# Kernel tuning notes

Measured on AMD Instinct MI355X. Metric: run time of the kernel, lower is better.

The kernel has to match this reference:

```python
import jax, jax.numpy as jnp
import numpy as np

BN_EPS = 1e-5


def _bn(x, gamma, beta):
    # training-mode BatchNorm1d: biased batch stats over the edge/batch axis
    mean = jnp.mean(x, axis=0, keepdims=True)
    var = jnp.mean((x - mean) ** 2, axis=0, keepdims=True)
    return (x - mean) * jax.lax.rsqrt(var + BN_EPS) * gamma + beta


def setup_inputs() -> dict:
    key = jax.random.key(0)
    ks = jax.random.split(key, 20)
    N, E = 20000, 300000
    in_drug, in_prot, hidden = 256, 512, 256
    h2 = 2 * hidden

    def u(k, shape, fan_in):
        b = 1.0 / np.sqrt(fan_in)
        return jax.random.uniform(k, shape, jnp.float32, -b, b)

    return {
        "x_drug": jax.random.normal(ks[0], (N, in_drug), jnp.float32),
        "x_prot": jax.random.normal(ks[1], (N, in_prot), jnp.float32),
        "edge_index": jax.random.randint(ks[2], (2, E), 0, N, jnp.int64),
        "W_src": u(ks[3], (hidden, in_drug), in_drug),
        "W_dst": u(ks[4], (hidden, in_prot), in_prot),
        "W_gate": u(ks[5], (h2, h2), h2),
        "b_gate": u(ks[6], (h2,), h2),
        "W1": u(ks[7], (hidden, h2), h2),
        "b1": u(ks[8], (hidden,), h2),
        "g1": jnp.ones((hidden,), jnp.float32),
        "be1": jnp.zeros((hidden,), jnp.float32),
        "W2": u(ks[9], (hidden, hidden), hidden),
        "b2": u(ks[10], (hidden,), hidden),
        "g2": jnp.ones((hidden,), jnp.float32),
        "be2": jnp.zeros((hidden,), jnp.float32),
        "W3": u(ks[11], (1, hidden), hidden),
        "b3": u(ks[12], (1,), hidden),
        "W_bil": u(ks[13], (1, hidden, hidden), hidden),
        "b_bil": u(ks[14], (1,), hidden),
    }


def reference(x_drug, x_prot, edge_index, W_src, W_dst, W_gate, b_gate,
              W1, b1, g1, be1, W2, b2, g2, be2, W3, b3, W_bil, b_bil):
    src, dst = edge_index[0], edge_index[1]
    h_src = x_drug[src] @ W_src.T            # [E, H]
    h_dst = x_prot[dst] @ W_dst.T            # [E, H]
    h_cat = jnp.concatenate([h_src, h_dst], axis=1)  # [E, 2H]
    gate = jax.nn.sigmoid(h_cat @ W_gate.T + b_gate)
    h = gate * h_cat
    # MLP (dropout is identity here)
    h1 = jax.nn.relu(_bn(h @ W1.T + b1, g1, be1))
    h2_ = jax.nn.relu(_bn(h1 @ W2.T + b2, g2, be2))
    mlp_score = (h2_ @ W3.T + b3).reshape(-1)
    # Bilinear: out_ek = sum_ij h_src_ei W_kij h_dst_ej + b_k
    bil_score = (jnp.einsum("ei,kij,ej->ek", h_src, W_bil, h_dst) + b_bil).reshape(-1)
    return mlp_score + bil_score
```

## Files before the change

### kernel.cpp

```cpp
#include <hip/hip_runtime.h>
#include <hip/hip_bf16.h>

typedef unsigned short u16;
typedef __attribute__((ext_vector_type(8))) short bf16x8;
typedef __attribute__((ext_vector_type(8))) unsigned short us8;
typedef __attribute__((ext_vector_type(4))) float f32x4;


__device__ __forceinline__ float b2f(u16 u) {
    union { unsigned u32; float f; } x; x.u32 = ((unsigned)u) << 16; return x.f;
}
__device__ __forceinline__ u16 f2b(float f) {
    union { float f; unsigned u; } x; x.f = f;
    unsigned r = x.u + 0x7fffu + ((x.u >> 16) & 1u);
    return (u16)(r >> 16);
}

__global__ __launch_bounds__(256) void zero_kernel(float* p, int n) {
    int i = blockIdx.x * 256 + threadIdx.x;
    if (i < n) p[i] = 0.f;
}

struct CvtSeg { const float* in; u16* out; int n4; };
struct CvtArr { CvtSeg s[6]; int tot4; };
__global__ __launch_bounds__(256) void cvt_fused(CvtArr ca) {
    int i = blockIdx.x * 256 + threadIdx.x;
    if (i >= ca.tot4) return;
    int k = 0, off = i;
#pragma unroll
    for (int q = 0; q < 6; ++q) {
        if (off < ca.s[q].n4) { k = q; break; }
        off -= ca.s[q].n4;
    }
    float4 v = ((const float4*)ca.s[k].in)[off];
    ushort4 o; o.x = f2b(v.x); o.y = f2b(v.y); o.z = f2b(v.z); o.w = f2b(v.w);
    ((ushort4*)ca.s[k].out)[off] = o;
}

struct GDesc {
    const void* A; int lda; int a_f32;
    const u16* W; int ldb;
    u16* C; int ldc;
    int K;
    const float* bias;
};
template <int NY> struct GDescArr { GDesc d[NY]; };

template <int NY>
__global__ __launch_bounds__(256, 2) void mfma_node(GDescArr<NY> da, int M)
{
    const GDesc dd = da.d[blockIdx.y];
    __shared__ u16 As[2][128][40];
    __shared__ u16 Bs[2][256][40];
    const int t = threadIdx.x;
    const int row0 = blockIdx.x * 128;
    const int arow = t >> 1, aks = (t & 1) * 16;
    const int agr = min(row0 + arow, M - 1);
    const int w = t >> 6, lane = t & 63;
    const int wr = w >> 1, wc = w & 1;
    const int lrow = lane & 15, lkg = lane >> 4;
    const int NIT = dd.K >> 5;

    f32x4 acc[4][8] = {};
    us8 ar[2], br[4];
    float4 fr[4];

    auto load_regs = [&](int it) {
        const int k0 = it << 5;
        if (dd.a_f32) {
            const float* ap = (const float*)dd.A + (size_t)agr * dd.lda + k0 + aks;
#pragma unroll
            for (int q = 0; q < 4; ++q) fr[q] = *(const float4*)(ap + q * 4);
        } else {
            const u16* ap = (const u16*)dd.A + (size_t)agr * dd.lda + k0 + aks;
            ar[0] = *(const us8*)ap; ar[1] = *(const us8*)(ap + 8);
        }
        const u16* wp = dd.W + (size_t)t * dd.ldb + k0;
#pragma unroll
        for (int q = 0; q < 4; ++q) br[q] = *(const us8*)(wp + q * 8);
    };
    auto proc_write = [&](int b) {
        if (dd.a_f32) {
#pragma unroll
            for (int q = 0; q < 2; ++q) {
                us8 o;
                const float fq[8] = {fr[q*2].x, fr[q*2].y, fr[q*2].z, fr[q*2].w,
                                     fr[q*2+1].x, fr[q*2+1].y, fr[q*2+1].z, fr[q*2+1].w};
#pragma unroll
                for (int j = 0; j < 8; ++j) o[j] = f2b(fq[j]);
                *(us8*)&As[b][arow][aks + q * 8] = o;
            }
        } else {
            *(us8*)&As[b][arow][aks] = ar[0];
            *(us8*)&As[b][arow][aks + 8] = ar[1];
        }
#pragma unroll
        for (int q = 0; q < 4; ++q) *(us8*)&Bs[b][t][q * 8] = br[q];
    };
    auto do_mfma = [&](int b) {
        bf16x8 af[4];
#pragma unroll
        for (int mi = 0; mi < 4; ++mi)
            af[mi] = *(const bf16x8*)&As[b][wr * 64 + mi * 16 + lrow][lkg * 8];
#pragma unroll
        for (int ni = 0; ni < 8; ++ni) {
            bf16x8 bfr = *(const bf16x8*)&Bs[b][wc * 128 + ni * 16 + lrow][lkg * 8];
#pragma unroll
            for (int mi = 0; mi < 4; ++mi)
                acc[mi][ni] = __builtin_amdgcn_mfma_f32_16x16x32_bf16(
                    af[mi], bfr, acc[mi][ni], 0, 0, 0);
        }
    };

    load_regs(0); proc_write(0); __syncthreads();
    for (int it = 0; it < NIT; ++it) {
        const int cur = it & 1;
        if (it + 1 < NIT) load_regs(it + 1);
        do_mfma(cur);
        if (it + 1 < NIT) proc_write(cur ^ 1);
        __syncthreads();
    }

#pragma unroll
    for (int ni = 0; ni < 8; ++ni) {
        const int gcol = wc * 128 + ni * 16 + lrow;
        const float bv = dd.bias ? dd.bias[gcol] : 0.f;
#pragma unroll
        for (int mi = 0; mi < 4; ++mi) {
            f32x4 v = acc[mi][ni];
#pragma unroll
            for (int j = 0; j < 4; ++j) {
                const int grow = row0 + wr * 64 + mi * 16 + lkg * 4 + j;
                if (grow < M) dd.C[(size_t)grow * dd.ldc + gcol] = f2b(v[j] + bv);
            }
        }
    }
}

#define OP_GATE   1
#define OP_BNRELU 2

template <int AOP>
__global__ __launch_bounds__(256) void mfma_edge(
    const u16* __restrict__ Ain,
    const u16* __restrict__ Wb, int ldb, int K,
    u16* __restrict__ C, int E,
    const int* __restrict__ ei,
    const u16* __restrict__ Gs, const u16* __restrict__ Gd,
    const u16* __restrict__ Hs, const u16* __restrict__ Hd,
    const u16* __restrict__ Bd, const float* __restrict__ b_bil,
    float* __restrict__ bil,
    const float* __restrict__ scaleK, const float* __restrict__ shiftK,
    float* __restrict__ sums)
{
    __shared__ u16 As[64][72];
    __shared__ u16 Bs[256][72];
    __shared__ float wsum[2][256];

    const int t = threadIdx.x;
    const int row0 = blockIdx.x * 64;
    const int arow = t >> 2;
    const int aks  = (t & 3) * 16;
    const int agr = min(row0 + arow, E - 1);

    int s_ = 0, d_ = 0;
    if constexpr (AOP == OP_GATE) { s_ = ei[agr]; d_ = ei[E + agr]; }

    const int lane = t & 63;
    const int wc = t >> 6;
    const int lrow = lane & 15, lkg = lane >> 4;
    const int NKS = K >> 6;

    f32x4 acc[4][4] = {};
    float bdot = 0.f;
    us8 aw0, aw1, br[8];

    auto loadA = [&](int ks) {
        const int k = ks * 64 + aks;
        if constexpr (AOP == OP_GATE) {
            us8 gs0 = *(const us8*)(Gs + (size_t)s_ * 512 + k);
            us8 gs1 = *(const us8*)(Gs + (size_t)s_ * 512 + k + 8);
            us8 gd0 = *(const us8*)(Gd + (size_t)d_ * 512 + k);
            us8 gd1 = *(const us8*)(Gd + (size_t)d_ * 512 + k + 8);
            const u16* hp = (ks < 4) ? (Hs + (size_t)s_ * 256 + k)
                                     : (Hd + (size_t)d_ * 256 + k - 256);
            us8 h0 = *(const us8*)hp, h1 = *(const us8*)(hp + 8);
#pragma unroll
            for (int j = 0; j < 8; ++j) {
                const float x0 = b2f(gs0[j]) + b2f(gd0[j]);
                const float x1 = b2f(gs1[j]) + b2f(gd1[j]);
                aw0[j] = f2b(b2f(h0[j]) / (1.f + __expf(-x0)));
                aw1[j] = f2b(b2f(h1[j]) / (1.f + __expf(-x1)));
            }
            if (ks < 4) {
                us8 bd0 = *(const us8*)(Bd + (size_t)d_ * 256 + k);
                us8 bd1 = *(const us8*)(Bd + (size_t)d_ * 256 + k + 8);
#pragma unroll
                for (int j = 0; j < 8; ++j) {
                    bdot = fmaf(b2f(h0[j]), b2f(bd0[j]), bdot);
                    bdot = fmaf(b2f(h1[j]), b2f(bd1[j]), bdot);
                }
            }
        } else {
            us8 a0 = *(const us8*)(Ain + (size_t)agr * 256 + k);
            us8 a1 = *(const us8*)(Ain + (size_t)agr * 256 + k + 8);
            float4 c0 = *(const float4*)(scaleK + k);
            float4 c1 = *(const float4*)(scaleK + k + 4);
            float4 c2 = *(const float4*)(scaleK + k + 8);
            float4 c3 = *(const float4*)(scaleK + k + 12);
            float4 h0 = *(const float4*)(shiftK + k);
            float4 h1 = *(const float4*)(shiftK + k + 4);
            float4 h2 = *(const float4*)(shiftK + k + 8);
            float4 h3 = *(const float4*)(shiftK + k + 12);
            const float scq[16] = {c0.x,c0.y,c0.z,c0.w, c1.x,c1.y,c1.z,c1.w,
                                   c2.x,c2.y,c2.z,c2.w, c3.x,c3.y,c3.z,c3.w};
            const float shq[16] = {h0.x,h0.y,h0.z,h0.w, h1.x,h1.y,h1.z,h1.w,
                                   h2.x,h2.y,h2.z,h2.w, h3.x,h3.y,h3.z,h3.w};
#pragma unroll
            for (int j = 0; j < 8; ++j) {
                aw0[j] = f2b(fmaxf(fmaf(b2f(a0[j]), scq[j],     shq[j]),     0.f));
                aw1[j] = f2b(fmaxf(fmaf(b2f(a1[j]), scq[8 + j], shq[8 + j]), 0.f));
            }
        }
    };
    auto loadB = [&](int ks) {
        const u16* wp = Wb + (size_t)t * ldb + ks * 64;
#pragma unroll
        for (int q = 0; q < 8; ++q) br[q] = *(const us8*)(wp + q * 8);
    };
    auto writeLDS = [&]() {
        *(us8*)&As[arow][aks]     = aw0;
        *(us8*)&As[arow][aks + 8] = aw1;
#pragma unroll
        for (int q = 0; q < 8; ++q) *(us8*)&Bs[t][q * 8] = br[q];
    };
    auto mfma_slab = [&]() {
#pragma unroll
        for (int kk = 0; kk < 64; kk += 32) {
            bf16x8 af[4], bf[4];
#pragma unroll
            for (int mi = 0; mi < 4; ++mi)
                af[mi] = *(const bf16x8*)&As[mi * 16 + lrow][kk + lkg * 8];
#pragma unroll
            for (int ni = 0; ni < 4; ++ni)
                bf[ni] = *(const bf16x8*)&Bs[wc * 64 + ni * 16 + lrow][kk + lkg * 8];
#pragma unroll
            for (int ni = 0; ni < 4; ++ni)
#pragma unroll
                for (int mi = 0; mi < 4; ++mi)
                    acc[mi][ni] = __builtin_amdgcn_mfma_f32_16x16x32_bf16(
                        af[mi], bf[ni], acc[mi][ni], 0, 0, 0);
        }
    };

    loadA(0); loadB(0);
    for (int ks = 0; ks < NKS; ++ks) {
        writeLDS();
        __syncthreads();
        if (ks + 1 < NKS) { loadA(ks + 1); loadB(ks + 1); }
        mfma_slab();
        __syncthreads();
    }

    if constexpr (AOP == OP_GATE) {
        bdot += __shfl_xor(bdot, 1, 64);
        bdot += __shfl_xor(bdot, 2, 64);
        if ((t & 3) == 0 && row0 + arow < E)
            bil[row0 + arow] = bdot + b_bil[0];
    }

#pragma unroll
    for (int ni = 0; ni < 4; ++ni) {
        const int gcol = wc * 64 + ni * 16 + lrow;
        float s = 0.f, ss = 0.f;
#pragma unroll
        for (int mi = 0; mi < 4; ++mi) {
            f32x4 v = acc[mi][ni];
#pragma unroll
            for (int j = 0; j < 4; ++j) {
                const int grow = row0 + mi * 16 + lkg * 4 + j;
                const float x = v[j];
                if (grow < E) {
                    C[(size_t)grow * 256 + gcol] = f2b(x);
                    s += x; ss = fmaf(x, x, ss);
                }
            }
        }
        s  += __shfl_xor(s, 16, 64);  s  += __shfl_xor(s, 32, 64);
        ss += __shfl_xor(ss, 16, 64); ss += __shfl_xor(ss, 32, 64);
        if (lkg == 0) { wsum[0][gcol] = s; wsum[1][gcol] = ss; }
    }
    __syncthreads();
    atomicAdd(&sums[t],       wsum[0][t]);
    atomicAdd(&sums[256 + t], wsum[1][t]);
}

__global__ void finalize_kernel(
    const float* __restrict__ sums, const float* __restrict__ g,
    const float* __restrict__ be, int M,
    float* __restrict__ scale, float* __restrict__ shift)
{
    const int c = threadIdx.x;
    const float inv = 1.f / (float)M;
    const float mean = sums[c] * inv;
    const float var  = sums[256 + c] * inv - mean * mean;
    const float sc = g[c] * rsqrtf(var + 1e-5f);
    scale[c] = sc;
    shift[c] = fmaf(-mean, sc, be[c]);
}

__global__ __launch_bounds__(256) void final_kernel(
    const u16* __restrict__ Z2,
    const float* __restrict__ scale2, const float* __restrict__ shift2,
    const float* __restrict__ W3, const float* __restrict__ b3,
    const float* __restrict__ bil,
    float* __restrict__ out, int E)
{
    const int w = threadIdx.x >> 6, lane = threadIdx.x & 63;
    const int e = blockIdx.x * 4 + w;
    if (e >= E) return;
    ushort4 zv = *(const ushort4*)(Z2 + (size_t)e * 256 + lane * 4);
    float4 sc = *(const float4*)(scale2 + lane * 4);
    float4 sh = *(const float4*)(shift2 + lane * 4);
    float4 w3 = *(const float4*)(W3 + lane * 4);
    const u16 zq[4] = {zv.x, zv.y, zv.z, zv.w};
    const float scq[4] = {sc.x, sc.y, sc.z, sc.w};
    const float shq[4] = {sh.x, sh.y, sh.z, sh.w};
    const float wq[4] = {w3.x, w3.y, w3.z, w3.w};
    float acc = 0.f;
#pragma unroll
    for (int i = 0; i < 4; ++i) {
        const float x = fmaxf(fmaf(b2f(zq[i]), scq[i], shq[i]), 0.f);
        acc = fmaf(x, wq[i], acc);
    }
#pragma unroll
    for (int off = 32; off; off >>= 1) acc += __shfl_down(acc, off, 64);
    if (lane == 0) out[e] = acc + b3[0] + bil[e];
}

extern "C" void kernel_launch(void* const* d_in, const int* in_sizes, int n_in,
                              void* d_out, int out_size, void* d_ws, size_t ws_size,
                              hipStream_t stream)
{
    const float* x_drug = (const float*)d_in[0];
    const float* x_prot = (const float*)d_in[1];
    const int*   ei     = (const int*)d_in[2];
    const float* W_src  = (const float*)d_in[3];
    const float* W_dst  = (const float*)d_in[4];
    const float* W_gate = (const float*)d_in[5];
    const float* b_gate = (const float*)d_in[6];
    const float* W1     = (const float*)d_in[7];
    const float* g1     = (const float*)d_in[9];
    const float* be1    = (const float*)d_in[10];
    const float* W2     = (const float*)d_in[11];
    const float* g2     = (const float*)d_in[13];
    const float* be2    = (const float*)d_in[14];
    const float* W3     = (const float*)d_in[15];
    const float* b3     = (const float*)d_in[16];
    const float* W_bil  = (const float*)d_in[17];
    const float* b_bil  = (const float*)d_in[18];
    float* out = (float*)d_out;

    const int N = in_sizes[0] / 256;
    const int E = in_sizes[2] / 2;

    char* wp_ = (char*)d_ws;
    auto alloc = [&](size_t bytes) {
        char* p = wp_; wp_ += (bytes + 255) & ~(size_t)255; return p;
    };
    u16* Wsrcb  = (u16*)alloc(256 * 256 * 2);
    u16* Wdstb  = (u16*)alloc(256 * 512 * 2);
    u16* Wgateb = (u16*)alloc(512 * 512 * 2);
    u16* Wbilb  = (u16*)alloc(256 * 256 * 2);
    u16* W1b    = (u16*)alloc(256 * 512 * 2);
    u16* W2b    = (u16*)alloc(256 * 256 * 2);
    u16* Hs     = (u16*)alloc((size_t)N * 256 * 2);
    u16* Hd     = (u16*)alloc((size_t)N * 256 * 2);
    u16* Gs     = (u16*)alloc((size_t)N * 512 * 2);
    u16* Gd     = (u16*)alloc((size_t)N * 512 * 2);
    u16* Bd     = (u16*)alloc((size_t)N * 256 * 2);
    u16* z      = (u16*)alloc((size_t)E * 256 * 2);
    float* bil  = (float*)alloc((size_t)E * 4);
    float* sums   = (float*)alloc(1024 * 4);
    float* scale1 = (float*)alloc(256 * 4);
    float* shift1 = (float*)alloc(256 * 4);
    float* scale2 = (float*)alloc(256 * 4);
    float* shift2 = (float*)alloc(256 * 4);

    zero_kernel<<<4, 256, 0, stream>>>(sums, 1024);

    CvtArr ca;
    ca.s[0] = {W_src,  Wsrcb,  256 * 256 / 4};
    ca.s[1] = {W_dst,  Wdstb,  256 * 512 / 4};
    ca.s[2] = {W_gate, Wgateb, 512 * 512 / 4};
    ca.s[3] = {W_bil,  Wbilb,  256 * 256 / 4};
    ca.s[4] = {W1,     W1b,    256 * 512 / 4};
    ca.s[5] = {W2,     W2b,    256 * 256 / 4};
    ca.tot4 = 0;
    for (int q = 0; q < 6; ++q) ca.tot4 += ca.s[q].n4;
    cvt_fused<<<(ca.tot4 + 255) / 256, 256, 0, stream>>>(ca);

    const int gxN = (N + 127) / 128;
    const int gxE = (E + 63) / 64;

    GDescArr<2> p1;
    p1.d[0] = {x_drug, 256, 1, Wsrcb, 256, Hs, 256, 256, nullptr};
    p1.d[1] = {x_prot, 512, 1, Wdstb, 512, Hd, 256, 512, nullptr};
    mfma_node<2><<<dim3(gxN, 2), 256, 0, stream>>>(p1, N);

    GDescArr<5> p2;
    p2.d[0] = {Hs, 256, 0, Wgateb,                 512, Gs,       512, 256, b_gate};
    p2.d[1] = {Hs, 256, 0, Wgateb + 256 * 512,     512, Gs + 256, 512, 256, b_gate + 256};
    p2.d[2] = {Hd, 256, 0, Wgateb + 256,           512, Gd,       512, 256, nullptr};
    p2.d[3] = {Hd, 256, 0, Wgateb + 256 * 512 + 256, 512, Gd + 256, 512, 256, nullptr};
    p2.d[4] = {Hd, 256, 0, Wbilb,                  256, Bd,       256, 256, nullptr};
    mfma_node<5><<<dim3(gxN, 5), 256, 0, stream>>>(p2, N);

    mfma_edge<OP_GATE><<<gxE, 256, 0, stream>>>(
        nullptr, W1b, 512, 512, z, E,
        ei, Gs, Gd, Hs, Hd, Bd, b_bil, bil, nullptr, nullptr, sums);
    finalize_kernel<<<1, 256, 0, stream>>>(sums, g1, be1, E, scale1, shift1);

    mfma_edge<OP_BNRELU><<<gxE, 256, 0, stream>>>(
        z, W2b, 256, 256, z, E,
        nullptr, nullptr, nullptr, nullptr, nullptr, nullptr, nullptr, nullptr,
        scale1, shift1, sums + 512);
    finalize_kernel<<<1, 256, 0, stream>>>(sums + 512, g2, be2, E, scale2, shift2);

    final_kernel<<<(E + 3) / 4, 256, 0, stream>>>(
        z, scale2, shift2, W3, b3, bil, out, E);
}
```

Measured before the change: 602.1 us.

## Load edge-GEMM weights directly to LDS with pre-swizzled layout

W1 and W2 are now repacked into a k-slab-major, XOR-swizzled bf16 layout so each 64-wide K slab is contiguous. The edge GEMM then streams B tiles with global_load_lds straight into LDS, skipping the register round trip, and reads them back with the matching swizzle to avoid bank conflicts. B loads are issued after the second barrier, which reorders the pipeline. The sigmoid division is replaced with a hardware reciprocal, trading a little precision for cheaper math.

New measurement: 525.7 us. 12.7% less time.

```diff
diff --git a/kernel.cpp b/kernel.cpp
--- a/kernel.cpp
+++ b/kernel.cpp
@@ -22,19 +22,31 @@
 }
 
 struct CvtSeg { const float* in; u16* out; int n4; };
-struct CvtArr { CvtSeg s[6]; int tot4; };
+struct CvtArr { CvtSeg s[4]; int tot4; };
 __global__ __launch_bounds__(256) void cvt_fused(CvtArr ca) {
     int i = blockIdx.x * 256 + threadIdx.x;
     if (i >= ca.tot4) return;
     int k = 0, off = i;
 #pragma unroll
-    for (int q = 0; q < 6; ++q) {
+    for (int q = 0; q < 4; ++q) {
         if (off < ca.s[q].n4) { k = q; break; }
         off -= ca.s[q].n4;
     }
     float4 v = ((const float4*)ca.s[k].in)[off];
     ushort4 o; o.x = f2b(v.x); o.y = f2b(v.y); o.z = f2b(v.z); o.w = f2b(v.w);
     ((ushort4*)ca.s[k].out)[off] = o;
+}
+
+__global__ __launch_bounds__(256) void repack_swz(const float* __restrict__ W,
+                                                  u16* __restrict__ out,
+                                                  int total, int kbits) {
+    int idx = blockIdx.x * 256 + threadIdx.x;
+    if (idx >= total) return;
+    const int n = idx >> kbits;
+    const int k = idx & ((1 << kbits) - 1);
+    const int ks = k >> 6, ke = k & 63;
+    const int j = ke ^ ((n & 7) << 3);
+    out[(((ks << 8) + n) << 6) + j] = f2b(W[idx]);
 }
 
 struct GDesc {
@@ -143,7 +155,7 @@
 template <int AOP>
 __global__ __launch_bounds__(256) void mfma_edge(
     const u16* __restrict__ Ain,
-    const u16* __restrict__ Wb, int ldb, int K,
+    const u16* __restrict__ Wb, int K,
     u16* __restrict__ C, int E,
     const int* __restrict__ ei,
     const u16* __restrict__ Gs, const u16* __restrict__ Gd,
@@ -154,7 +166,7 @@
     float* __restrict__ sums)
 {
     __shared__ u16 As[64][72];
-    __shared__ u16 Bs[256][72];
+    __shared__ u16 Bs[256 * 64];
     __shared__ float wsum[2][256];
 
     const int t = threadIdx.x;
@@ -167,13 +179,13 @@
     if constexpr (AOP == OP_GATE) { s_ = ei[agr]; d_ = ei[E + agr]; }
 
     const int lane = t & 63;
-    const int wc = t >> 6;
+    const int w = t >> 6;
     const int lrow = lane & 15, lkg = lane >> 4;
     const int NKS = K >> 6;
 
     f32x4 acc[4][4] = {};
     float bdot = 0.f;
-    us8 aw0, aw1, br[8];
+    us8 aw0, aw1;
 
     auto loadA = [&](int ks) {
         const int k = ks * 64 + aks;
@@ -189,8 +201,10 @@
             for (int j = 0; j < 8; ++j) {
                 const float x0 = b2f(gs0[j]) + b2f(gd0[j]);
                 const float x1 = b2f(gs1[j]) + b2f(gd1[j]);
-                aw0[j] = f2b(b2f(h0[j]) / (1.f + __expf(-x0)));
-                aw1[j] = f2b(b2f(h1[j]) / (1.f + __expf(-x1)));
+                const float r0 = __builtin_amdgcn_rcpf(1.f + __expf(-x0));
+                const float r1 = __builtin_amdgcn_rcpf(1.f + __expf(-x1));
+                aw0[j] = f2b(b2f(h0[j]) * r0);
+                aw1[j] = f2b(b2f(h1[j]) * r1);
             }
             if (ks < 4) {
                 us8 bd0 = *(const us8*)(Bd + (size_t)d_ * 256 + k);
@@ -223,16 +237,19 @@
             }
         }
     };
-    auto loadB = [&](int ks) {
-        const u16* wp = Wb + (size_t)t * ldb + ks * 64;
-#pragma unroll
-        for (int q = 0; q < 8; ++q) br[q] = *(const us8*)(wp + q * 8);
-    };
-    auto writeLDS = [&]() {
+    auto writeA = [&]() {
         *(us8*)&As[arow][aks]     = aw0;
         *(us8*)&As[arow][aks + 8] = aw1;
-#pragma unroll
-        for (int q = 0; q < 8; ++q) *(us8*)&Bs[t][q * 8] = br[q];
+    };
+    auto gloadB = [&](int ks) {
+        const char* g = (const char*)(Wb + ((size_t)ks << 14)) + w * 8192 + lane * 16;
+        char* l = (char*)Bs + w * 8192;
+#pragma unroll
+        for (int q = 0; q < 8; ++q)
+            __builtin_amdgcn_global_load_lds(
+                (const __attribute__((address_space(1))) unsigned int*)(g + q * 1024),
+                (__attribute__((address_space(3))) unsigned int*)(l + q * 1024),
+                16, 0, 0);
     };
     auto mfma_slab = [&]() {
 #pragma unroll
@@ -242,8 +259,10 @@
             for (int mi = 0; mi < 4; ++mi)
                 af[mi] = *(const bf16x8*)&As[mi * 16 + lrow][kk + lkg * 8];
 #pragma unroll
-            for (int ni = 0; ni < 4; ++ni)
-                bf[ni] = *(const bf16x8*)&Bs[wc * 64 + ni * 16 + lrow][kk + lkg * 8];
+            for (int ni = 0; ni < 4; ++ni) {
+                const int r = w * 64 + ni * 16 + lrow;
+                bf[ni] = *(const bf16x8*)&Bs[r * 64 + ((kk + lkg * 8) ^ ((r & 7) << 3))];
+            }
 #pragma unroll
             for (int ni = 0; ni < 4; ++ni)
 #pragma unroll
@@ -253,13 +272,14 @@
         }
     };
 
-    loadA(0); loadB(0);
+    gloadB(0); loadA(0);
     for (int ks = 0; ks < NKS; ++ks) {
-        writeLDS();
+        writeA();
         __syncthreads();
-        if (ks + 1 < NKS) { loadA(ks + 1); loadB(ks + 1); }
+        if (ks + 1 < NKS) loadA(ks + 1);
         mfma_slab();
         __syncthreads();
+        if (ks + 1 < NKS) gloadB(ks + 1);
     }
 
     if constexpr (AOP == OP_GATE) {
@@ -271,7 +291,7 @@
 
 #pragma unroll
     for (int ni = 0; ni < 4; ++ni) {
-        const int gcol = wc * 64 + ni * 16 + lrow;
+        const int gcol = w * 64 + ni * 16 + lrow;
         float s = 0.f, ss = 0.f;
 #pragma unroll
         for (int mi = 0; mi < 4; ++mi) {
@@ -372,8 +392,8 @@
     u16* Wdstb  = (u16*)alloc(256 * 512 * 2);
     u16* Wgateb = (u16*)alloc(512 * 512 * 2);
     u16* Wbilb  = (u16*)alloc(256 * 256 * 2);
-    u16* W1b    = (u16*)alloc(256 * 512 * 2);
-    u16* W2b    = (u16*)alloc(256 * 256 * 2);
+    u16* W1s    = (u16*)alloc(256 * 512 * 2);
+    u16* W2s    = (u16*)alloc(256 * 256 * 2);
     u16* Hs     = (u16*)alloc((size_t)N * 256 * 2);
     u16* Hd     = (u16*)alloc((size_t)N * 256 * 2);
     u16* Gs     = (u16*)alloc((size_t)N * 512 * 2);
@@ -394,11 +414,12 @@
     ca.s[1] = {W_dst,  Wdstb,  256 * 512 / 4};
     ca.s[2] = {W_gate, Wgateb, 512 * 512 / 4};
     ca.s[3] = {W_bil,  Wbilb,  256 * 256 / 4};
-    ca.s[4] = {W1,     W1b,    256 * 512 / 4};
-    ca.s[5] = {W2,     W2b,    256 * 256 / 4};
     ca.tot4 = 0;
-    for (int q = 0; q < 6; ++q) ca.tot4 += ca.s[q].n4;
+    for (int q = 0; q < 4; ++q) ca.tot4 += ca.s[q].n4;
     cvt_fused<<<(ca.tot4 + 255) / 256, 256, 0, stream>>>(ca);
+
+    repack_swz<<<(256 * 512 + 255) / 256, 256, 0, stream>>>(W1, W1s, 256 * 512, 9);
+    repack_swz<<<(256 * 256 + 255) / 256, 256, 0, stream>>>(W2, W2s, 256 * 256, 8);
 
     const int gxN = (N + 127) / 128;
     const int gxE = (E + 63) / 64;
@@ -417,12 +438,12 @@
     mfma_node<5><<<dim3(gxN, 5), 256, 0, stream>>>(p2, N);
 
     mfma_edge<OP_GATE><<<gxE, 256, 0, stream>>>(
-        nullptr, W1b, 512, 512, z, E,
+        nullptr, W1s, 512, z, E,
         ei, Gs, Gd, Hs, Hd, Bd, b_bil, bil, nullptr, nullptr, sums);
     finalize_kernel<<<1, 256, 0, stream>>>(sums, g1, be1, E, scale1, shift1);
 
     mfma_edge<OP_BNRELU><<<gxE, 256, 0, stream>>>(
-        z, W2b, 256, 256, z, E,
+        z, W2s, 256, z, E,
         nullptr, nullptr, nullptr, nullptr, nullptr, nullptr, nullptr, nullptr,
         scale1, shift1, sums + 512);
     finalize_kernel<<<1, 256, 0, stream>>>(sums + 512, g2, be2, E, scale2, shift2);
```
